# Performance work log

Measured on AMD Instinct MI355X. Metric: run time of the kernel, lower is better.

The kernel has to match this reference:

```python
import jax, jax.numpy as jnp
import numpy as np

N, L, H, D = 2, 2048, 8, 64
DIM = H * D  # 512
P = 1  # position_dimension


def setup_inputs() -> dict:
    key = jax.random.key(0)
    ks = jax.random.split(key, 7)
    y = jax.random.normal(ks[0], (N, L, DIM), dtype=jnp.float32)
    # token positions, shape (N, L, P)
    positions = jnp.broadcast_to(
        jnp.arange(L, dtype=jnp.float32)[None, :, None], (N, L, P))
    scale = 0.02
    Wq = jax.random.normal(ks[1], (DIM, DIM), dtype=jnp.float32) * scale
    Wk = jax.random.normal(ks[2], (DIM, DIM), dtype=jnp.float32) * scale
    Wv = jax.random.normal(ks[3], (DIM, DIM), dtype=jnp.float32) * scale
    position_coeffs = jnp.ones((H, D), dtype=jnp.float32)
    # small so cos(pq - pk) stays near 1 and scaled scores are well-conditioned
    position_weight = jax.random.normal(ks[4], (H, D, P), dtype=jnp.float32) * 0.01
    position_bias = jax.random.normal(ks[5], (H, D), dtype=jnp.float32) * 0.01
    return {"y": y, "positions": positions, "Wq": Wq, "Wk": Wk, "Wv": Wv,
            "position_coeffs": position_coeffs,
            "position_weight": position_weight,
            "position_bias": position_bias}


def reference(y, positions, Wq, Wk, Wv, position_coeffs, position_weight,
              position_bias):
    n, l, _ = y.shape
    # QKV projections; kernel_function (softplus, i.e. log(1+exp)) on q and k
    q = jax.nn.softplus(y @ Wq.T).reshape(n, l, H, D).transpose(0, 2, 1, 3)
    k = jax.nn.softplus(y @ Wk.T).reshape(n, l, H, D).transpose(0, 2, 1, 3)
    v = (y @ Wv.T).reshape(n, l, H, D).transpose(0, 2, 1, 3)
    # projected positions pq = pk : (N, H, L, D)
    p = jnp.einsum('hdp,nlp->nhld', position_weight, positions) \
        + position_bias[None, :, None, :]
    cos_p, sin_p = jnp.cos(p), jnp.sin(p)
    # score_ij = sum_d q_d k_d c_d (cos pq_d cos pk_d + sin pq_d sin pk_d)
    coeff = position_coeffs[None, :, None, :]
    qc, kc = q * coeff * cos_p, k * cos_p
    qs, ks = q * coeff * sin_p, k * sin_p
    score = jnp.einsum('nhqd,nhkd->nhqk', qc, kc) \
          + jnp.einsum('nhqd,nhkd->nhqk', qs, ks)
    # mask_future (future_offset = 0): zero out keys j > i
    causal = jnp.tril(jnp.ones((l, l), dtype=bool))
    score = jnp.where(causal[None, None], score, 0.0)
    # scaled: scores sum to 1 along keys
    score = score / jnp.sum(score, axis=-1, keepdims=True)
    att = jnp.einsum('nhqk,nhkd->nhqd', score, v)
    return att.transpose(0, 2, 1, 3).reshape(n, l, DIM)
```

## Files before the change

### kernel.cpp

```cpp
#include <hip/hip_runtime.h>
#include <hip/hip_bf16.h>

typedef __attribute__((ext_vector_type(8))) short bf16x8;
typedef __attribute__((ext_vector_type(4))) float f32x4;
typedef unsigned int u32;

#define L_SEQ 2048
#define NHEAD 8
#define DHEAD 64
#define DMODEL 512
#define QK_STRIDE 262144
#define V_STRIDE  131072

__device__ __forceinline__ short f2bf(float f) {
    union { float f; unsigned u; } x; x.f = f;
    unsigned r = x.u + 0x7FFFu + ((x.u >> 16) & 1u);
    return (short)(r >> 16);
}

__device__ __forceinline__ void split1(float x, short& hi, short& lo) {
    unsigned uh = __float_as_uint(x) & 0xFFFF0000u;
    hi = (short)(uh >> 16);
    lo = f2bf(x - __uint_as_float(uh));
}

__device__ __forceinline__ void split8(const float* p, bf16x8& hi, bf16x8& lo) {
    #pragma unroll
    for (int i = 0; i < 8; ++i) {
        float x = p[i];
        unsigned uh = __float_as_uint(x) & 0xFFFF0000u;
        hi[i] = (short)(uh >> 16);
        lo[i] = f2bf(x - __uint_as_float(uh));
    }
}

__device__ __forceinline__ u32 cvtpk_bf16(float a, float b) {
    u32 r;
    asm("v_cvt_pk_bf16_f32 %0, %1, %2" : "=v"(r) : "v"(a), "v"(b));
    return r;
}

__device__ __forceinline__ void gload_lds16(const void* g, void* l) {
    __builtin_amdgcn_global_load_lds(
        (const __attribute__((address_space(1))) unsigned int*)g,
        (__attribute__((address_space(3))) unsigned int*)l, 16, 0, 0);
}

__global__ __launch_bounds__(256) void split_kernel(
    const float* __restrict__ y,
    const float* __restrict__ Wq, const float* __restrict__ Wk, const float* __restrict__ Wv,
    short* __restrict__ yh, short* __restrict__ yl,
    short* __restrict__ wh, short* __restrict__ wl)
{
    const int wv = threadIdx.x >> 6, ln = threadIdx.x & 63;
    const int u = blockIdx.x * 4 + wv;
    float tmp[8];
    if (u < 4096) {
        const int B = u >> 4, kb = u & 15;
        const int row = B*16 + (ln & 15);
        const int k   = kb*32 + (ln >> 4)*8;
        const float* src = y + (size_t)row * DMODEL + k;
        *(float4*)tmp       = *(const float4*)src;
        *(float4*)(tmp + 4) = *(const float4*)(src + 4);
        bf16x8 hi, lo;
        split8(tmp, hi, lo);
        const size_t dst = (size_t)u*512 + ln*8;
        *(bf16x8*)(yh + dst) = hi;
        *(bf16x8*)(yl + dst) = lo;
    } else {
        const int u2 = u - 4096;
        const int mat = u2 >> 9;
        const int r   = u2 & 511;
        const int C = r >> 4, kb = r & 15;
        const float* W = (mat == 0) ? Wq : (mat == 1) ? Wk : Wv;
        const int col = C*16 + (ln & 15);
        const int k   = kb*32 + (ln >> 4)*8;
        const float* src = W + (size_t)col * DMODEL + k;
        *(float4*)tmp       = *(const float4*)src;
        *(float4*)(tmp + 4) = *(const float4*)(src + 4);
        bf16x8 hi, lo;
        split8(tmp, hi, lo);
        const size_t dst = (size_t)u2*512 + ln*8;
        *(bf16x8*)(wh + dst) = hi;
        *(bf16x8*)(wl + dst) = lo;
    }
}

__global__ __launch_bounds__(256) void prep_kernel(
    const short* __restrict__ yh, const short* __restrict__ yl,
    const short* __restrict__ wh, const short* __restrict__ wl,
    const float* __restrict__ positions,
    const float* __restrict__ coeff, const float* __restrict__ pw, const float* __restrict__ pb,
    short* __restrict__ Qh, short* __restrict__ Ql,
    short* __restrict__ Kh, short* __restrict__ Kl,
    short* __restrict__ Vh, short* __restrict__ Vl)
{
    __shared__ float vtile[128][65];
    const int mode = blockIdx.z;
    const int m_base = blockIdx.x * 128;
    const int h = blockIdx.y;
    const int n_base = h * 64;
    const int tid = threadIdx.x;
    const int lane = tid & 63;
    const int wv = tid >> 6;
    const int lr = lane & 15;
    const int lg = lane >> 4;

    const short* whm = wh + (size_t)mode * 262144;
    const short* wlm = wl + (size_t)mode * 262144;
    const int Ba0 = blockIdx.x*8 + wv*2;

    f32x4 acc[2][4];
    #pragma unroll
    for (int t = 0; t < 2; ++t)
        #pragma unroll
        for (int c = 0; c < 4; ++c) acc[t][c] = (f32x4){0.f, 0.f, 0.f, 0.f};

    #pragma unroll 4
    for (int kb = 0; kb < 16; ++kb) {
        bf16x8 ah[2], al[2], bh[4], bl[4];
        #pragma unroll
        for (int t = 0; t < 2; ++t) {
            const size_t off = ((size_t)((Ba0 + t)*16 + kb)*64 + lane)*8;
            ah[t] = *(const bf16x8*)(yh + off);
            al[t] = *(const bf16x8*)(yl + off);
        }
        #pragma unroll
        for (int c = 0; c < 4; ++c) {
            const size_t off = ((size_t)((h*4 + c)*16 + kb)*64 + lane)*8;
            bh[c] = *(const bf16x8*)(whm + off);
            bl[c] = *(const bf16x8*)(wlm + off);
        }
        #pragma unroll
        for (int t = 0; t < 2; ++t)
            #pragma unroll
            for (int c = 0; c < 4; ++c) {
                acc[t][c] = __builtin_amdgcn_mfma_f32_16x16x32_bf16(ah[t], bh[c], acc[t][c], 0, 0, 0);
                acc[t][c] = __builtin_amdgcn_mfma_f32_16x16x32_bf16(ah[t], bl[c], acc[t][c], 0, 0, 0);
                acc[t][c] = __builtin_amdgcn_mfma_f32_16x16x32_bf16(al[t], bh[c], acc[t][c], 0, 0, 0);
            }
    }

    const int n_idx = m_base >> 11;
    const int nh = n_idx * NHEAD + h;

    if (mode == 2) {
        #pragma unroll
        for (int t = 0; t < 2; ++t)
            #pragma unroll
            for (int c = 0; c < 4; ++c)
                #pragma unroll
                for (int r = 0; r < 4; ++r)
                    vtile[wv*32 + t*16 + lg*4 + r][c*16 + lr] = acc[t][c][r];
        __syncthreads();
        const size_t vbase = (size_t)nh * V_STRIDE;
        #pragma unroll
        for (int i = 0; i < 32; ++i) {
            const int key_l = (tid & 7) + 8*(i & 15);
            const int d     = (tid >> 3) + 32*(i >> 4);
            const int key   = (m_base & (L_SEQ - 1)) + key_l;
            short th, tl;
            split1(vtile[key_l][d], th, tl);
            const size_t idx = vbase +
                ((size_t)((key >> 5)*4 + (d >> 4))*64 + (d & 15) + 16*((key >> 3) & 3))*8 + (key & 7);
            Vh[idx] = th; Vl[idx] = tl;
        }
    } else {
        short* OUTh = (mode == 0) ? Qh : Kh;
        short* OUTl = (mode == 0) ? Ql : Kl;
        const size_t qbase_nh = (size_t)nh * QK_STRIDE;
        #pragma unroll
        for (int t = 0; t < 2; ++t) {
            #pragma unroll
            for (int c = 0; c < 4; ++c) {
                const int d = c*16 + lr;
                const float pwv = pw[n_base + d];
                const float pbv = pb[n_base + d];
                const float cf  = (mode == 0) ? coeff[n_base + d] : 1.0f;
                const int lane_t = 16*((2*c + (lr >> 3)) & 3);
                const int j = lr & 7;
                #pragma unroll
                for (int r = 0; r < 4; ++r) {
                    const int gm = m_base + wv*32 + t*16 + lg*4 + r;
                    const int l = gm & (L_SEQ - 1);
                    const int B = l >> 4;
                    const float posv = positions[gm];
                    const float x = acc[t][c][r];
                    const float sp = fmaxf(x, 0.f) + __logf(1.f + __expf(-fabsf(x)));
                    const float p = pwv * posv + pbv;
                    const float cs = __cosf(p), sn = __sinf(p);
                    short h1, l1, h2, l2;
                    split1(sp * cf * cs, h1, l1);
                    split1(sp * cf * sn, h2, l2);
                    const int ln = (l & 15) + lane_t;
                    const size_t idx_c = qbase_nh + ((size_t)(B*4 + (c >> 1))*64 + ln)*8 + j;
                    const size_t idx_s = qbase_nh + ((size_t)(B*4 + 2 + (c >> 1))*64 + ln)*8 + j;
                    OUTh[idx_c] = h1; OUTl[idx_c] = l1;
                    OUTh[idx_s] = h2; OUTl[idx_s] = l2;
                }
            }
        }
    }
}

template<int CHUNK>
__global__ __launch_bounds__(256) void attn_kernel(
    const short* __restrict__ Qh, const short* __restrict__ Ql,
    const short* __restrict__ Kh, const short* __restrict__ Kl,
    const short* __restrict__ Vh, const short* __restrict__ Vl,
    float* __restrict__ O_part, float* __restrict__ rs_part)
{
    __shared__ char s_lds[49152];
    const int id = blockIdx.x;
    const int nh   = (id & 7)*2 + ((id >> 3) & 1);
    const int slot = id >> 4;

    int rem = slot, qt = 0;
    for (qt = 0; qt < 16; ++qt) {
        const int nch = (2*qt + 2 + CHUNK - 1) / CHUNK;
        if (rem < nch) break;
        rem -= nch;
    }
    const int nst = 2*qt + 2;
    const int kt0 = rem * CHUNK;
    const int kt1 = (kt0 + CHUNK < nst) ? (kt0 + CHUNK) : nst;

    const int q_base = qt * 128;
    const int tid = threadIdx.x;
    const int lane = tid & 63;
    const int wv = tid >> 6;
    const int lr = lane & 15;
    const int lg = lane >> 4;

    const short* Qh_b = Qh + (size_t)nh * QK_STRIDE;
    const short* Ql_b = Ql + (size_t)nh * QK_STRIDE;
    const short* Kh_b = Kh + (size_t)nh * QK_STRIDE;
    const short* Kl_b = Kl + (size_t)nh * QK_STRIDE;
    const short* Vh_b = Vh + (size_t)nh * V_STRIDE;
    const short* Vl_b = Vl + (size_t)nh * V_STRIDE;

    bf16x8 qh[2][4], ql[2][4];
    #pragma unroll
    for (int t = 0; t < 2; ++t) {
        const int Bq = qt*8 + wv*2 + t;
        #pragma unroll
        for (int kh = 0; kh < 4; ++kh) {
            const size_t off = ((size_t)(Bq*4 + kh)*64 + lane)*8;
            qh[t][kh] = *(const bf16x8*)(Qh_b + off);
            ql[t][kh] = *(const bf16x8*)(Ql_b + off);
        }
    }

    f32x4 o_acc[2][4];
    float rs[2];
    #pragma unroll
    for (int t = 0; t < 2; ++t) {
        #pragma unroll
        for (int c = 0; c < 4; ++c) o_acc[t][c] = (f32x4){0.f, 0.f, 0.f, 0.f};
        rs[t] = 0.f;
    }

    const int addr0 = (lr + ((lg & 1) * 2) * 16) << 2;
    const int addr1 = addr0 + 64;
    const bool selhi = (lg >= 2);
    const int lb = lane << 4;

    for (int kt = kt0; kt < kt1; ++kt) {
        {
            const char* kh_src = (const char*)(Kh_b + (size_t)kt*8192);
            const char* kl_src = (const char*)(Kl_b + (size_t)kt*8192);
            const char* vh_src = (const char*)(Vh_b + (size_t)kt*4096);
            const char* vl_src = (const char*)(Vl_b + (size_t)kt*4096);
            #pragma unroll
            for (int i = 0; i < 12; ++i) {
                const int ch = wv*12 + i;
                const char* src;
                if (ch < 16)      src = kh_src + ch*1024;
                else if (ch < 32) src = kl_src + (ch-16)*1024;
                else if (ch < 40) src = vh_src + (ch-32)*1024;
                else              src = vl_src + (ch-40)*1024;
                gload_lds16(src + lb, s_lds + ch*1024);
            }
        }
        __syncthreads();

        f32x4 st[2][4];
        #pragma unroll
        for (int t = 0; t < 2; ++t)
            #pragma unroll
            for (int c = 0; c < 4; ++c) st[t][c] = (f32x4){0.f, 0.f, 0.f, 0.f};

        #pragma unroll
        for (int c = 0; c < 4; ++c) {
            #pragma unroll
            for (int kh = 0; kh < 4; ++kh) {
                const int boff = (c*4 + kh)*1024 + lb;
                const bf16x8 kfh = *(const bf16x8*)(s_lds + boff);
                const bf16x8 kfl = *(const bf16x8*)(s_lds + 16384 + boff);
                #pragma unroll
                for (int t = 0; t < 2; ++t) {
                    st[t][c] = __builtin_amdgcn_mfma_f32_16x16x32_bf16(kfh, qh[t][kh], st[t][c], 0, 0, 0);
                    st[t][c] = __builtin_amdgcn_mfma_f32_16x16x32_bf16(kfh, ql[t][kh], st[t][c], 0, 0, 0);
                    st[t][c] = __builtin_amdgcn_mfma_f32_16x16x32_bf16(kfl, qh[t][kh], st[t][c], 0, 0, 0);
                }
            }
        }

        const int k0 = kt * 64;
        const bool domask = (kt >= 2*qt);
        #pragma unroll
        for (int t = 0; t < 2; ++t) {
            const int gq = q_base + wv*32 + t*16 + lr;
            float part = 0.f;
            #pragma unroll
            for (int c = 0; c < 4; ++c)
                #pragma unroll
                for (int r = 0; r < 4; ++r) {
                    const int gk = k0 + c*16 + lg*4 + r;
                    float v = st[t][c][r];
                    if (domask && gk > gq) v = 0.f;
                    st[t][c][r] = v;
                    part += v;
                }
            part += __shfl_xor(part, 16);
            part += __shfl_xor(part, 32);
            rs[t] += part;
        }

        u32 pwh[2][4][2], pwl[2][4][2];
        #pragma unroll
        for (int t = 0; t < 2; ++t)
            #pragma unroll
            for (int c = 0; c < 4; ++c) {
                const u32 b0 = __float_as_uint(st[t][c][0]);
                const u32 b1 = __float_as_uint(st[t][c][1]);
                const u32 b2 = __float_as_uint(st[t][c][2]);
                const u32 b3 = __float_as_uint(st[t][c][3]);
                pwh[t][c][0] = (b1 & 0xFFFF0000u) | (b0 >> 16);
                pwh[t][c][1] = (b3 & 0xFFFF0000u) | (b2 >> 16);
                const float l0 = st[t][c][0] - __uint_as_float(b0 & 0xFFFF0000u);
                const float l1 = st[t][c][1] - __uint_as_float(b1 & 0xFFFF0000u);
                const float l2 = st[t][c][2] - __uint_as_float(b2 & 0xFFFF0000u);
                const float l3 = st[t][c][3] - __uint_as_float(b3 & 0xFFFF0000u);
                pwl[t][c][0] = cvtpk_bf16(l0, l1);
                pwl[t][c][1] = cvtpk_bf16(l2, l3);
            }

        #pragma unroll
        for (int kc = 0; kc < 2; ++kc) {
            union { u32 u[4]; bf16x8 v; } pah[2], pal[2];
            #pragma unroll
            for (int t = 0; t < 2; ++t) {
                u32 a, b;
                a = (u32)__builtin_amdgcn_ds_bpermute(addr0, (int)pwh[t][2*kc][0]);
                b = (u32)__builtin_amdgcn_ds_bpermute(addr0, (int)pwh[t][2*kc+1][0]);
                pah[t].u[0] = selhi ? b : a;
                a = (u32)__builtin_amdgcn_ds_bpermute(addr0, (int)pwh[t][2*kc][1]);
                b = (u32)__builtin_amdgcn_ds_bpermute(addr0, (int)pwh[t][2*kc+1][1]);
                pah[t].u[1] = selhi ? b : a;
                a = (u32)__builtin_amdgcn_ds_bpermute(addr1, (int)pwh[t][2*kc][0]);
                b = (u32)__builtin_amdgcn_ds_bpermute(addr1, (int)pwh[t][2*kc+1][0]);
                pah[t].u[2] = selhi ? b : a;
                a = (u32)__builtin_amdgcn_ds_bpermute(addr1, (int)pwh[t][2*kc][1]);
                b = (u32)__builtin_amdgcn_ds_bpermute(addr1, (int)pwh[t][2*kc+1][1]);
                pah[t].u[3] = selhi ? b : a;

                a = (u32)__builtin_amdgcn_ds_bpermute(addr0, (int)pwl[t][2*kc][0]);
                b = (u32)__builtin_amdgcn_ds_bpermute(addr0, (int)pwl[t][2*kc+1][0]);
                pal[t].u[0] = selhi ? b : a;
                a = (u32)__builtin_amdgcn_ds_bpermute(addr0, (int)pwl[t][2*kc][1]);
                b = (u32)__builtin_amdgcn_ds_bpermute(addr0, (int)pwl[t][2*kc+1][1]);
                pal[t].u[1] = selhi ? b : a;
                a = (u32)__builtin_amdgcn_ds_bpermute(addr1, (int)pwl[t][2*kc][0]);
                b = (u32)__builtin_amdgcn_ds_bpermute(addr1, (int)pwl[t][2*kc+1][0]);
                pal[t].u[2] = selhi ? b : a;
                a = (u32)__builtin_amdgcn_ds_bpermute(addr1, (int)pwl[t][2*kc][1]);
                b = (u32)__builtin_amdgcn_ds_bpermute(addr1, (int)pwl[t][2*kc+1][1]);
                pal[t].u[3] = selhi ? b : a;
            }
            #pragma unroll
            for (int cd = 0; cd < 4; ++cd) {
                const int voff = (kc*4 + cd)*1024 + lb;
                const bf16x8 vfh = *(const bf16x8*)(s_lds + 32768 + voff);
                const bf16x8 vfl = *(const bf16x8*)(s_lds + 40960 + voff);
                #pragma unroll
                for (int t = 0; t < 2; ++t) {
                    o_acc[t][cd] = __builtin_amdgcn_mfma_f32_16x16x32_bf16(pah[t].v, vfh, o_acc[t][cd], 0, 0, 0);
                    o_acc[t][cd] = __builtin_amdgcn_mfma_f32_16x16x32_bf16(pah[t].v, vfl, o_acc[t][cd], 0, 0, 0);
                    o_acc[t][cd] = __builtin_amdgcn_mfma_f32_16x16x32_bf16(pal[t].v, vfh, o_acc[t][cd], 0, 0, 0);
                }
            }
        }
        __syncthreads();
    }

    const size_t slab = (size_t)slot * 16 + nh;
    #pragma unroll
    for (int t = 0; t < 2; ++t)
        if (lg == 0)
            rs_part[slab*128 + wv*32 + t*16 + lr] = rs[t];

    #pragma unroll
    for (int t = 0; t < 2; ++t)
        #pragma unroll
        for (int cd = 0; cd < 4; ++cd)
            #pragma unroll
            for (int r = 0; r < 4; ++r) {
                const int row = wv*32 + t*16 + lg*4 + r;
                O_part[slab*8192 + row*64 + cd*16 + lr] = o_acc[t][cd][r];
            }
}

template<int CHUNK>
__global__ __launch_bounds__(256) void reduce_div_kernel(
    const float* __restrict__ O_part, const float* __restrict__ rs_part,
    float* __restrict__ out)
{
    const int idx = blockIdx.x * 256 + threadIdx.x;
    const int d4 = idx & 15;
    const int l  = (idx >> 4) & (L_SEQ - 1);
    const int nh = idx >> 15;
    const int qt = l >> 7;
    const int row = l & 127;
    int cs = 0;
    for (int q = 0; q < qt; ++q) cs += (2*q + 2 + CHUNK - 1) / CHUNK;
    const int nch = (2*qt + 2 + CHUNK - 1) / CHUNK;

    float4 o = {0.f, 0.f, 0.f, 0.f};
    float rssum = 0.f;
    for (int ci = 0; ci < nch; ++ci) {
        const size_t slab = (size_t)(cs + ci) * 16 + nh;
        const float4 p = *(const float4*)(O_part + slab*8192 + row*64 + d4*4);
        o.x += p.x; o.y += p.y; o.z += p.z; o.w += p.w;
        rssum += rs_part[slab*128 + row];
    }
    const float inv = 1.0f / rssum;
    float4 r;
    r.x = o.x * inv; r.y = o.y * inv; r.z = o.z * inv; r.w = o.w * inv;
    const int n = nh >> 3, h = nh & 7;
    *(float4*)(out + ((size_t)(n*L_SEQ + l))*DMODEL + h*DHEAD + d4*4) = r;
}

extern "C" void kernel_launch(void* const* d_in, const int* in_sizes, int n_in,
                              void* d_out, int out_size, void* d_ws, size_t ws_size,
                              hipStream_t stream) {
    const float* y         = (const float*)d_in[0];
    const float* positions = (const float*)d_in[1];
    const float* Wq        = (const float*)d_in[2];
    const float* Wk        = (const float*)d_in[3];
    const float* Wv        = (const float*)d_in[4];
    const float* coeff     = (const float*)d_in[5];
    const float* pw        = (const float*)d_in[6];
    const float* pb        = (const float*)d_in[7];
    float* out = (float*)d_out;

    const size_t SQK = (size_t)16 * QK_STRIDE;
    const size_t SV  = (size_t)16 * V_STRIDE;
    const size_t SY  = (size_t)4096 * 512;
    const size_t SW  = (size_t)3 * 512 * 512;
    short* Qh = (short*)d_ws;
    short* Ql = Qh + SQK;
    short* Kh = Ql + SQK;
    short* Kl = Kh + SQK;
    short* Vh = Kl + SQK;
    short* Vl = Vh + SV;
    short* yh = Vl + SV;
    short* yl = yh + SY;
    short* wh = yl + SY;
    short* wl = wh + SW;
    float* O_part = (float*)(wl + SW);
    const size_t base_bytes = (SQK*4 + SV*2 + SY*2 + SW*2) * sizeof(short);
    const size_t per_slot   = (size_t)16 * (8192 + 128) * sizeof(float);

    split_kernel<<<dim3(1408), dim3(256), 0, stream>>>(y, Wq, Wk, Wv, yh, yl, wh, wl);
    prep_kernel<<<dim3(32, 8, 3), dim3(256), 0, stream>>>(
        yh, yl, wh, wl, positions, coeff, pw, pb, Qh, Ql, Kh, Kl, Vh, Vl);

    if (ws_size >= base_bytes + 136 * per_slot) {
        float* rs_part = O_part + (size_t)136 * 16 * 8192;
        attn_kernel<2><<<dim3(136 * 16), dim3(256), 0, stream>>>(
            Qh, Ql, Kh, Kl, Vh, Vl, O_part, rs_part);
        reduce_div_kernel<2><<<dim3(2048), dim3(256), 0, stream>>>(O_part, rs_part, out);
    } else if (ws_size >= base_bytes + 72 * per_slot) {
        float* rs_part = O_part + (size_t)72 * 16 * 8192;
        attn_kernel<4><<<dim3(72 * 16), dim3(256), 0, stream>>>(
            Qh, Ql, Kh, Kl, Vh, Vl, O_part, rs_part);
        reduce_div_kernel<4><<<dim3(2048), dim3(256), 0, stream>>>(O_part, rs_part, out);
    } else {
        float* rs_part = O_part + (size_t)40 * 16 * 8192;
        attn_kernel<8><<<dim3(40 * 16), dim3(256), 0, stream>>>(
            Qh, Ql, Kh, Kl, Vh, Vl, O_part, rs_part);
        reduce_div_kernel<8><<<dim3(2048), dim3(256), 0, stream>>>(O_part, rs_part, out);
    }
}
```

Measured before the change: 113.5 us.

## Double-buffer K tiles in LDS, load V directly to registers, use CHUNK=4

The attention kernel now prefetches the next key tile's K hi/lo into a second LDS buffer while the current tile is computed, and removes the barrier that previously waited on each tile's load. V fragments are read straight from global memory into registers instead of being staged through LDS. LDS per block grows to 64 KB, and the CHUNK=2 path is dropped so the default uses CHUNK=4 with fewer, longer-running blocks. The aim is to hide global load latency, at the cost of less LDS occupancy, more registers, and fewer split blocks to balance the causal work.

New measurement: 101.5 us. 1.12x faster.

```diff
diff --git a/kernel.cpp b/kernel.cpp
--- a/kernel.cpp
+++ b/kernel.cpp
@@ -210,7 +210,7 @@
     const short* __restrict__ Vh, const short* __restrict__ Vl,
     float* __restrict__ O_part, float* __restrict__ rs_part)
 {
-    __shared__ char s_lds[49152];
+    __shared__ char s_lds[65536];
     const int id = blockIdx.x;
     const int nh   = (id & 7)*2 + ((id >> 3) & 1);
     const int slot = id >> 4;
@@ -265,25 +265,43 @@
     const bool selhi = (lg >= 2);
     const int lb = lane << 4;
 
+    {
+        const char* kh_src = (const char*)(Kh_b + (size_t)kt0*8192);
+        const char* kl_src = (const char*)(Kl_b + (size_t)kt0*8192);
+        #pragma unroll
+        for (int i = 0; i < 8; ++i) {
+            const int ch = wv*8 + i;
+            const char* src = (ch < 16) ? kh_src + ch*1024 : kl_src + (ch-16)*1024;
+            gload_lds16(src + lb, s_lds + ch*1024);
+        }
+    }
+    __syncthreads();
+
+    int cur = 0;
     for (int kt = kt0; kt < kt1; ++kt) {
-        {
-            const char* kh_src = (const char*)(Kh_b + (size_t)kt*8192);
-            const char* kl_src = (const char*)(Kl_b + (size_t)kt*8192);
-            const char* vh_src = (const char*)(Vh_b + (size_t)kt*4096);
-            const char* vl_src = (const char*)(Vl_b + (size_t)kt*4096);
-            #pragma unroll
-            for (int i = 0; i < 12; ++i) {
-                const int ch = wv*12 + i;
-                const char* src;
-                if (ch < 16)      src = kh_src + ch*1024;
-                else if (ch < 32) src = kl_src + (ch-16)*1024;
-                else if (ch < 40) src = vh_src + (ch-32)*1024;
-                else              src = vl_src + (ch-40)*1024;
-                gload_lds16(src + lb, s_lds + ch*1024);
-            }
-        }
-        __syncthreads();
-
+        if (kt + 1 < kt1) {
+            const char* kh_src = (const char*)(Kh_b + (size_t)(kt+1)*8192);
+            const char* kl_src = (const char*)(Kl_b + (size_t)(kt+1)*8192);
+            char* dst = s_lds + (cur ? 0 : 32768);
+            #pragma unroll
+            for (int i = 0; i < 8; ++i) {
+                const int ch = wv*8 + i;
+                const char* src = (ch < 16) ? kh_src + ch*1024 : kl_src + (ch-16)*1024;
+                gload_lds16(src + lb, dst + ch*1024);
+            }
+        }
+
+        bf16x8 vfh[2][4], vfl[2][4];
+        #pragma unroll
+        for (int kc = 0; kc < 2; ++kc)
+            #pragma unroll
+            for (int cd = 0; cd < 4; ++cd) {
+                const size_t voff = ((size_t)((kt*2 + kc)*4 + cd)*64 + lane)*8;
+                vfh[kc][cd] = *(const bf16x8*)(Vh_b + voff);
+                vfl[kc][cd] = *(const bf16x8*)(Vl_b + voff);
+            }
+
+        const char* kbuf = s_lds + (cur ? 32768 : 0);
         f32x4 st[2][4];
         #pragma unroll
         for (int t = 0; t < 2; ++t)
@@ -295,8 +313,8 @@
             #pragma unroll
             for (int kh = 0; kh < 4; ++kh) {
                 const int boff = (c*4 + kh)*1024 + lb;
-                const bf16x8 kfh = *(const bf16x8*)(s_lds + boff);
-                const bf16x8 kfl = *(const bf16x8*)(s_lds + 16384 + boff);
+                const bf16x8 kfh = *(const bf16x8*)(kbuf + boff);
+                const bf16x8 kfl = *(const bf16x8*)(kbuf + 16384 + boff);
                 #pragma unroll
                 for (int t = 0; t < 2; ++t) {
                     st[t][c] = __builtin_amdgcn_mfma_f32_16x16x32_bf16(kfh, qh[t][kh], st[t][c], 0, 0, 0);
@@ -380,18 +398,16 @@
             }
             #pragma unroll
             for (int cd = 0; cd < 4; ++cd) {
-                const int voff = (kc*4 + cd)*1024 + lb;
-                const bf16x8 vfh = *(const bf16x8*)(s_lds + 32768 + voff);
-                const bf16x8 vfl = *(const bf16x8*)(s_lds + 40960 + voff);
                 #pragma unroll
                 for (int t = 0; t < 2; ++t) {
-                    o_acc[t][cd] = __builtin_amdgcn_mfma_f32_16x16x32_bf16(pah[t].v, vfh, o_acc[t][cd], 0, 0, 0);
-                    o_acc[t][cd] = __builtin_amdgcn_mfma_f32_16x16x32_bf16(pah[t].v, vfl, o_acc[t][cd], 0, 0, 0);
-                    o_acc[t][cd] = __builtin_amdgcn_mfma_f32_16x16x32_bf16(pal[t].v, vfh, o_acc[t][cd], 0, 0, 0);
+                    o_acc[t][cd] = __builtin_amdgcn_mfma_f32_16x16x32_bf16(pah[t].v, vfh[kc][cd], o_acc[t][cd], 0, 0, 0);
+                    o_acc[t][cd] = __builtin_amdgcn_mfma_f32_16x16x32_bf16(pah[t].v, vfl[kc][cd], o_acc[t][cd], 0, 0, 0);
+                    o_acc[t][cd] = __builtin_amdgcn_mfma_f32_16x16x32_bf16(pal[t].v, vfh[kc][cd], o_acc[t][cd], 0, 0, 0);
                 }
             }
         }
         __syncthreads();
+        cur ^= 1;
     }
 
     const size_t slab = (size_t)slot * 16 + nh;
@@ -476,12 +492,7 @@
     prep_kernel<<<dim3(32, 8, 3), dim3(256), 0, stream>>>(
         yh, yl, wh, wl, positions, coeff, pw, pb, Qh, Ql, Kh, Kl, Vh, Vl);
 
-    if (ws_size >= base_bytes + 136 * per_slot) {
-        float* rs_part = O_part + (size_t)136 * 16 * 8192;
-        attn_kernel<2><<<dim3(136 * 16), dim3(256), 0, stream>>>(
-            Qh, Ql, Kh, Kl, Vh, Vl, O_part, rs_part);
-        reduce_div_kernel<2><<<dim3(2048), dim3(256), 0, stream>>>(O_part, rs_part, out);
-    } else if (ws_size >= base_bytes + 72 * per_slot) {
+    if (ws_size >= base_bytes + 72 * per_slot) {
         float* rs_part = O_part + (size_t)72 * 16 * 8192;
         attn_kernel<4><<<dim3(72 * 16), dim3(256), 0, stream>>>(
             Qh, Ql, Kh, Kl, Vh, Vl, O_part, rs_part);
```
